# Kernel optimization log

Hardware: AMD Instinct MI355X
Metric: run time of the kernel (lower is better)

The kernel has to match this reference:

```python
import jax, jax.numpy as jnp
import numpy as np

N = 16384   # nodes
E = 524288  # edges (avg degree 32)
D = 32      # input_dim == output_dim


def setup_inputs() -> dict:
    key = jax.random.key(0)
    k_x, k_e, k_wa, k_ba, k_wu, k_bu = jax.random.split(key, 6)
    x = jax.random.normal(k_x, (N, D), dtype=jnp.float32)
    edge_index = jax.random.randint(k_e, (2, E), 0, N, dtype=jnp.int32)
    # nn.Linear init: U(-1/sqrt(fan_in), 1/sqrt(fan_in)), weight shape [out, in]
    bound = 1.0 / np.sqrt(D)
    W_agg = jax.random.uniform(k_wa, (D, D), jnp.float32, -bound, bound)
    b_agg = jax.random.uniform(k_ba, (D,), jnp.float32, -bound, bound)
    W_upd = jax.random.uniform(k_wu, (D, D), jnp.float32, -bound, bound)
    b_upd = jax.random.uniform(k_bu, (D,), jnp.float32, -bound, bound)
    return {"x": x, "edge_index": edge_index, "W_agg": W_agg, "b_agg": b_agg,
            "W_upd": W_upd, "b_upd": b_upd}


def reference(x, edge_index, W_agg, b_agg, W_upd, b_upd):
    n = x.shape[0]
    src, dst = edge_index[0], edge_index[1]
    # Dense symmetric 0/1 adjacency, exactly as the torch module builds it
    # (duplicate edges still write 1 via .set, matching index_put semantics).
    adj = jnp.zeros((n, n), dtype=x.dtype)
    adj = adj.at[src, dst].set(1.0)
    adj = adj.at[dst, src].set(1.0)
    messages = adj @ x                              # [N, D]
    aggregated = messages @ W_agg.T + b_agg         # aggregate_fn(messages)
    updated = x @ W_upd.T + b_upd + aggregated      # update_fn(x) + aggregated
    return updated
```

## Files before the change

kernel.cpp:

```cpp
#include <hip/hip_runtime.h>

#define D 32
#define GCAP 256

__global__ void gnn_edge_bits(const int* __restrict__ src,
                              const int* __restrict__ dst,
                              unsigned int* __restrict__ bm,
                              int E, int wpr) {
    int e = blockIdx.x * blockDim.x + threadIdx.x;
    if (e >= E) return;
    int s = src[e];
    int d = dst[e];
    atomicOr(&bm[(size_t)d * wpr + (s >> 5)], 1u << (s & 31));
    atomicOr(&bm[(size_t)s * wpr + (d >> 5)], 1u << (d & 31));
}

__global__ __launch_bounds__(256) void gnn_gather_update(
        const unsigned int* __restrict__ bm,
        const float* __restrict__ x,
        float* __restrict__ out,
        const float* __restrict__ W_agg,
        const float* __restrict__ b_agg,
        const float* __restrict__ W_upd,
        const float* __restrict__ b_upd,
        int wpr) {
    __shared__ float sWa[D][D + 1];
    __shared__ float sWu[D][D + 1];
    __shared__ float sbias[D];
    __shared__ float sx[16][D];
    __shared__ float sm[16][D];
    __shared__ int   slist[4][4][GCAP];

    int t = threadIdx.x;
    for (int i = t; i < D * D; i += 256) {
        sWa[i >> 5][i & 31] = W_agg[i];
        sWu[i >> 5][i & 31] = W_upd[i];
    }
    if (t < D) sbias[t] = b_agg[t] + b_upd[t];
    for (int i = t; i < 16 * D; i += 256)
        ((float*)sx)[i] = x[(size_t)blockIdx.x * 16 * D + i];

    int lane = t & 63;
    int wv   = t >> 6;
    int dim  = lane & 31;
    int half = lane >> 5;
    int nb   = blockIdx.x * 16 + wv * 4;

    uint4 q[8];
#pragma unroll
    for (int nn = 0; nn < 4; ++nn) {
        const uint4* row = (const uint4*)(bm + (size_t)(nb + nn) * wpr);
        q[nn * 2 + 0] = row[lane];
        q[nn * 2 + 1] = row[64 + lane];
    }

    float accs[4];
#pragma unroll
    for (int nn = 0; nn < 4; ++nn) {
        unsigned int w[8] = { q[nn*2].x,   q[nn*2].y,   q[nn*2].z,   q[nn*2].w,
                              q[nn*2+1].x, q[nn*2+1].y, q[nn*2+1].z, q[nn*2+1].w };
        int myc = 0;
#pragma unroll
        for (int k = 0; k < 8; ++k) myc += __popc(w[k]);
        int pre = myc;
#pragma unroll
        for (int off = 1; off < 64; off <<= 1) {
            int v = __shfl_up(pre, off, 64);
            if (lane >= off) pre += v;
        }
        int total = __shfl(pre, 63, 64);
        pre -= myc;

        float acc = 0.f;
        if (total <= GCAP) {
            int p = pre;
#pragma unroll
            for (int k = 0; k < 8; ++k) {
                unsigned int ww = w[k];
                int widx = (k < 4) ? (4 * lane + k) : (256 + 4 * lane + k - 4);
                int base = widx * 32;
                while (ww) {
                    int b = __ffs(ww) - 1;
                    ww &= ww - 1;
                    slist[wv][nn][p++] = base + b;
                }
            }
            __asm__ __volatile__("s_waitcnt lgkmcnt(0)" ::: "memory");

            const int* sl = slist[wv][nn];
            int j = half;
            for (; j + 16 <= total; j += 16) {
                int c0 = sl[j +  0], c1 = sl[j +  2], c2 = sl[j +  4], c3 = sl[j +  6];
                int c4 = sl[j +  8], c5 = sl[j + 10], c6 = sl[j + 12], c7 = sl[j + 14];
                float v0 = x[(size_t)c0 * D + dim];
                float v1 = x[(size_t)c1 * D + dim];
                float v2 = x[(size_t)c2 * D + dim];
                float v3 = x[(size_t)c3 * D + dim];
                float v4 = x[(size_t)c4 * D + dim];
                float v5 = x[(size_t)c5 * D + dim];
                float v6 = x[(size_t)c6 * D + dim];
                float v7 = x[(size_t)c7 * D + dim];
                acc += v0; acc += v1; acc += v2; acc += v3;
                acc += v4; acc += v5; acc += v6; acc += v7;
            }
            for (; j < total; j += 2)
                acc += x[(size_t)sl[j] * D + dim];
        } else {
#pragma unroll
            for (int k = 0; k < 8; ++k) {
                unsigned long long m = __ballot(w[k] != 0);
                while (m) {
                    int l = __ffsll(m) - 1;
                    m &= m - 1;
                    unsigned int ww = __shfl(w[k], l, 64);
                    int widx = (k < 4) ? (4 * l + k) : (256 + 4 * l + k - 4);
                    int base = widx * 32;
                    while (ww) {
                        int b = __ffs(ww) - 1;
                        ww &= ww - 1;
                        acc += x[(size_t)(base + b) * D + dim];
                    }
                }
            }
        }
        accs[nn] = acc;
    }

#pragma unroll
    for (int nn = 0; nn < 4; ++nn) {
        float a = accs[nn] + __shfl_xor(accs[nn], 32, 64);
        if (lane < D) sm[wv * 4 + nn][lane] = a;
    }
    __syncthreads();

    for (int o = t; o < 16 * D; o += 256) {
        int nl = o >> 5, od = o & 31;
        float r = sbias[od];
#pragma unroll
        for (int k = 0; k < D; ++k)
            r += sx[nl][k] * sWu[od][k] + sm[nl][k] * sWa[od][k];
        out[((size_t)blockIdx.x * 16 + nl) * D + od] = r;
    }
}

#define HASH_BITS 20
#define HASH_SIZE (1u << HASH_BITS)
#define EMPTY_KEY 0xFFFFFFFFu

__global__ void gnn_edge_scatter(const int* __restrict__ src,
                                 const int* __restrict__ dst,
                                 const float* __restrict__ x,
                                 float* __restrict__ msg,
                                 unsigned int* __restrict__ htab, int E, int N) {
    int e = blockIdx.x * blockDim.x + threadIdx.x;
    if (e >= E) return;
    int s = src[e], d = dst[e];
    int a = s < d ? s : d, b = s < d ? d : s;
    unsigned long long key = (unsigned long long)a * N + b;
    unsigned int k32 = (unsigned int)(key & 0xFFFFFFFEu) | 1u;
    unsigned int h = ((unsigned int)key * 2654435761u) >> (32 - HASH_BITS);
    bool inserted;
    for (;;) {
        unsigned int prev = atomicCAS(&htab[h], EMPTY_KEY, k32);
        if (prev == EMPTY_KEY) { inserted = true; break; }
        if (prev == k32)       { inserted = false; break; }
        h = (h + 1) & (HASH_SIZE - 1);
    }
    if (!inserted) return;
    const float* xs = x + (size_t)s * D;
    const float* xd = x + (size_t)d * D;
    if (s == d) {
        float* m = msg + (size_t)s * D;
#pragma unroll
        for (int i = 0; i < D; ++i) atomicAdd(&m[i], xs[i]);
    } else {
        float* ms = msg + (size_t)s * D;
        float* md = msg + (size_t)d * D;
#pragma unroll
        for (int i = 0; i < D; ++i) {
            atomicAdd(&ms[i], xd[i]);
            atomicAdd(&md[i], xs[i]);
        }
    }
}

__global__ __launch_bounds__(256) void gnn_update(
        const float* __restrict__ x, float* __restrict__ out,
        const float* __restrict__ W_agg, const float* __restrict__ b_agg,
        const float* __restrict__ W_upd, const float* __restrict__ b_upd) {
    __shared__ float sWa[D][D + 1], sWu[D][D + 1], sb[D];
    __shared__ float sx[8][D], sm[8][D];
    int t = threadIdx.x;
    for (int i = t; i < D * D; i += 256) {
        sWa[i >> 5][i & 31] = W_agg[i];
        sWu[i >> 5][i & 31] = W_upd[i];
    }
    if (t < D) sb[t] = b_agg[t] + b_upd[t];
    int g = t >> 5, o = t & 31;
    size_t node = (size_t)blockIdx.x * 8 + g;
    sx[g][o] = x[node * D + o];
    sm[g][o] = out[node * D + o];
    __syncthreads();
    float acc = sb[o];
#pragma unroll
    for (int k = 0; k < D; ++k)
        acc += sx[g][k] * sWu[o][k] + sm[g][k] * sWa[o][k];
    out[node * D + o] = acc;
}


extern "C" void kernel_launch(void* const* d_in, const int* in_sizes, int n_in,
                              void* d_out, int out_size, void* d_ws, size_t ws_size,
                              hipStream_t stream) {
    const float* x     = (const float*)d_in[0];
    const int*   eidx  = (const int*)d_in[1];
    const float* W_agg = (const float*)d_in[2];
    const float* b_agg = (const float*)d_in[3];
    const float* W_upd = (const float*)d_in[4];
    const float* b_upd = (const float*)d_in[5];
    float* out = (float*)d_out;

    const int E = in_sizes[1] / 2;
    const int N = in_sizes[0] / D;
    const int* src = eidx;
    const int* dst = eidx + E;

    const int wpr = N >> 5;
    const size_t bm_bytes = (size_t)N * wpr * sizeof(unsigned int);

    if ((N & 15) == 0 && ws_size >= bm_bytes) {
        unsigned int* bm = (unsigned int*)d_ws;
        hipMemsetAsync(bm, 0, bm_bytes, stream);
        gnn_edge_bits<<<(E + 255) / 256, 256, 0, stream>>>(src, dst, bm, E, wpr);
        gnn_gather_update<<<N / 16, 256, 0, stream>>>(bm, x, out, W_agg, b_agg,
                                                      W_upd, b_upd, wpr);
    } else {
        unsigned int* htab = (unsigned int*)d_ws;
        hipMemsetAsync(out, 0, (size_t)N * D * sizeof(float), stream);
        hipMemsetAsync(htab, 0xFF, (size_t)HASH_SIZE * sizeof(unsigned int), stream);
        gnn_edge_scatter<<<(E + 255) / 256, 256, 0, stream>>>(src, dst, x, out,
                                                              htab, E, N);
        gnn_update<<<N / 8, 256, 0, stream>>>(x, out, W_agg, b_agg, W_upd, b_upd);
    }
}
```

Before: 147.2 us.

## Fuse bitmap zero, edge scatter and gather into one cooperative kernel

Replaces the memset plus two kernel launches with a single cooperative kernel of 1024 blocks. It zeroes the adjacency bitmap, sets the edge bits with atomics, then gathers and applies the update, using grid-wide syncs between phases. The goal is to remove launch gaps and the memset. In exchange it adds grid barrier costs and fixes the grid size, which must fit co-resident on the device (N hardcoded to 16384). It also reworks the fallback path into smaller 4-node blocks.

```diff
diff --git a/kernel.cpp b/kernel.cpp
--- a/kernel.cpp
+++ b/kernel.cpp
@@ -1,60 +1,67 @@
 #include <hip/hip_runtime.h>
+#include <hip/hip_cooperative_groups.h>
+
+namespace cg = cooperative_groups;
 
 #define D 32
 #define GCAP 256
-
-__global__ void gnn_edge_bits(const int* __restrict__ src,
-                              const int* __restrict__ dst,
-                              unsigned int* __restrict__ bm,
-                              int E, int wpr) {
-    int e = blockIdx.x * blockDim.x + threadIdx.x;
-    if (e >= E) return;
-    int s = src[e];
-    int d = dst[e];
-    atomicOr(&bm[(size_t)d * wpr + (s >> 5)], 1u << (s & 31));
-    atomicOr(&bm[(size_t)s * wpr + (d >> 5)], 1u << (d & 31));
-}
-
-__global__ __launch_bounds__(256) void gnn_gather_update(
-        const unsigned int* __restrict__ bm,
-        const float* __restrict__ x,
-        float* __restrict__ out,
-        const float* __restrict__ W_agg,
-        const float* __restrict__ b_agg,
-        const float* __restrict__ W_upd,
-        const float* __restrict__ b_upd,
-        int wpr) {
-    __shared__ float sWa[D][D + 1];
-    __shared__ float sWu[D][D + 1];
-    __shared__ float sbias[D];
-    __shared__ float sx[16][D];
-    __shared__ float sm[16][D];
-    __shared__ int   slist[4][4][GCAP];
+#define FBLK 1024
+#define FTHR 256
+
+__global__ __launch_bounds__(FTHR, 4) void gnn_fused(
+        const int* __restrict__ src, const int* __restrict__ dst, int E,
+        unsigned int* __restrict__ bm, int wpr, int nwords,
+        const float* __restrict__ x, float* __restrict__ out,
+        const float* __restrict__ W_agg, const float* __restrict__ b_agg,
+        const float* __restrict__ W_upd, const float* __restrict__ b_upd) {
+    cg::grid_group grid = cg::this_grid();
+
+    __shared__ float sWa[D][D + 1], sWu[D][D + 1], sbias[D];
+    __shared__ float sx[16][D], sm[16][D];
+    __shared__ int   slist[4][GCAP];
 
     int t = threadIdx.x;
-    for (int i = t; i < D * D; i += 256) {
+    int gtid = blockIdx.x * FTHR + t;
+    const int T = FBLK * FTHR;
+
+    for (int i = t; i < D * D; i += FTHR) {
         sWa[i >> 5][i & 31] = W_agg[i];
         sWu[i >> 5][i & 31] = W_upd[i];
     }
     if (t < D) sbias[t] = b_agg[t] + b_upd[t];
-    for (int i = t; i < 16 * D; i += 256)
-        ((float*)sx)[i] = x[(size_t)blockIdx.x * 16 * D + i];
-
-    int lane = t & 63;
-    int wv   = t >> 6;
-    int dim  = lane & 31;
-    int half = lane >> 5;
-    int nb   = blockIdx.x * 16 + wv * 4;
+
+    uint4* bm4 = (uint4*)bm;
+    int nq = nwords >> 2;
+    uint4 z = make_uint4(0u, 0u, 0u, 0u);
+    for (int i = gtid; i < nq; i += T) bm4[i] = z;
+
+    __threadfence();
+    grid.sync();
+
+    for (int e = gtid; e < E; e += T) {
+        int s = src[e], d2 = dst[e];
+        atomicOr(&bm[(size_t)d2 * wpr + (s >> 5)], 1u << (s & 31));
+        atomicOr(&bm[(size_t)s * wpr + (d2 >> 5)], 1u << (d2 & 31));
+    }
+
+    __threadfence();
+    grid.sync();
+    __threadfence();
+
+    int lane = t & 63, wv = t >> 6, dim = lane & 31, half = lane >> 5;
+    int nb0 = blockIdx.x * 16;
+
+    for (int i = t; i < 16 * D; i += FTHR)
+        ((float*)sx)[i] = x[(size_t)nb0 * D + i];
 
     uint4 q[8];
 #pragma unroll
     for (int nn = 0; nn < 4; ++nn) {
-        const uint4* row = (const uint4*)(bm + (size_t)(nb + nn) * wpr);
-        q[nn * 2 + 0] = row[lane];
-        q[nn * 2 + 1] = row[64 + lane];
-    }
-
-    float accs[4];
+        const uint4* row4 = (const uint4*)(bm + (size_t)(nb0 + wv * 4 + nn) * wpr);
+        q[nn * 2 + 0] = row4[lane];
+        q[nn * 2 + 1] = row4[64 + lane];
+    }
+
 #pragma unroll
     for (int nn = 0; nn < 4; ++nn) {
         unsigned int w[8] = { q[nn*2].x,   q[nn*2].y,   q[nn*2].z,   q[nn*2].w,
@@ -82,12 +89,12 @@
                 while (ww) {
                     int b = __ffs(ww) - 1;
                     ww &= ww - 1;
-                    slist[wv][nn][p++] = base + b;
+                    slist[wv][p++] = base + b;
                 }
             }
             __asm__ __volatile__("s_waitcnt lgkmcnt(0)" ::: "memory");
 
-            const int* sl = slist[wv][nn];
+            const int* sl = slist[wv];
             int j = half;
             for (; j + 16 <= total; j += 16) {
                 int c0 = sl[j +  0], c1 = sl[j +  2], c2 = sl[j +  4], c3 = sl[j +  6];
@@ -123,24 +130,129 @@
                 }
             }
         }
-        accs[nn] = acc;
-    }
-
-#pragma unroll
-    for (int nn = 0; nn < 4; ++nn) {
-        float a = accs[nn] + __shfl_xor(accs[nn], 32, 64);
-        if (lane < D) sm[wv * 4 + nn][lane] = a;
+        acc += __shfl_xor(acc, 32, 64);
+        if (lane < D) sm[wv * 4 + nn][lane] = acc;
     }
     __syncthreads();
 
-    for (int o = t; o < 16 * D; o += 256) {
+    for (int o = t; o < 16 * D; o += FTHR) {
         int nl = o >> 5, od = o & 31;
         float r = sbias[od];
 #pragma unroll
         for (int k = 0; k < D; ++k)
             r += sx[nl][k] * sWu[od][k] + sm[nl][k] * sWa[od][k];
-        out[((size_t)blockIdx.x * 16 + nl) * D + od] = r;
-    }
+        out[((size_t)nb0 + nl) * D + od] = r;
+    }
+}
+
+__global__ void gnn_edge_bits(const int* __restrict__ src,
+                              const int* __restrict__ dst,
+                              unsigned int* __restrict__ bm,
+                              int E, int wpr) {
+    int e = blockIdx.x * blockDim.x + threadIdx.x;
+    if (e >= E) return;
+    int s = src[e];
+    int d = dst[e];
+    atomicOr(&bm[(size_t)d * wpr + (s >> 5)], 1u << (s & 31));
+    atomicOr(&bm[(size_t)s * wpr + (d >> 5)], 1u << (d & 31));
+}
+
+__global__ __launch_bounds__(256) void gnn_gather_update(
+        const unsigned int* __restrict__ bm,
+        const float* __restrict__ x,
+        float* __restrict__ out,
+        const float* __restrict__ W_agg,
+        const float* __restrict__ b_agg,
+        const float* __restrict__ W_upd,
+        const float* __restrict__ b_upd,
+        int wpr) {
+    __shared__ float sWa[D][D + 1];
+    __shared__ float sWu[D][D + 1];
+    __shared__ float sb[D];
+    __shared__ float sx[4][D];
+    __shared__ float sm[4][D];
+    __shared__ int   slist[4][384];
+
+    int t = threadIdx.x;
+    for (int i = t; i < D * D; i += 256) {
+        sWa[i >> 5][i & 31] = W_agg[i];
+        sWu[i >> 5][i & 31] = W_upd[i];
+    }
+    if (t < D) sb[t] = b_agg[t] + b_upd[t];
+
+    int lane = t & 63, wv = t >> 6, dim = lane & 31, half = lane >> 5;
+    size_t node = (size_t)blockIdx.x * 4 + wv;
+    if (lane < D) sx[wv][lane] = x[node * D + lane];
+
+    const unsigned int* row = bm + node * (size_t)wpr;
+    unsigned int wb[8];
+#pragma unroll
+    for (int c = 0; c < 8; ++c) wb[c] = row[c * 64 + lane];
+
+    int myc = 0;
+#pragma unroll
+    for (int c = 0; c < 8; ++c) myc += __popc(wb[c]);
+    int pre = myc;
+#pragma unroll
+    for (int off = 1; off < 64; off <<= 1) {
+        int v = __shfl_up(pre, off, 64);
+        if (lane >= off) pre += v;
+    }
+    int total = __shfl(pre, 63, 64);
+    pre -= myc;
+
+    float acc = 0.f;
+    if (total <= 384) {
+        int p = pre;
+#pragma unroll
+        for (int c = 0; c < 8; ++c) {
+            unsigned int ww = wb[c];
+            int base = (c * 64 + lane) * 32;
+            while (ww) { int b = __ffs(ww) - 1; ww &= ww - 1; slist[wv][p++] = base + b; }
+        }
+        __asm__ __volatile__("s_waitcnt lgkmcnt(0)" ::: "memory");
+        int j = half;
+        for (; j + 8 <= total; j += 8) {
+            int c0 = slist[wv][j + 0], c1 = slist[wv][j + 2];
+            int c2 = slist[wv][j + 4], c3 = slist[wv][j + 6];
+            float v0 = x[(size_t)c0 * D + dim];
+            float v1 = x[(size_t)c1 * D + dim];
+            float v2 = x[(size_t)c2 * D + dim];
+            float v3 = x[(size_t)c3 * D + dim];
+            acc += v0; acc += v1; acc += v2; acc += v3;
+        }
+        for (; j < total; j += 2) acc += x[(size_t)slist[wv][j] * D + dim];
+    } else {
+        for (int c = 0; c < 8; ++c) {
+            unsigned long long m = __ballot(wb[c] != 0);
+            while (m) {
+                int l = __ffsll(m) - 1; m &= m - 1;
+                unsigned int ww = __shfl(wb[c], l, 64);
+                int base = (c * 64 + l) * 32;
+                while (ww) { int b = __ffs(ww) - 1; ww &= ww - 1;
+                             acc += x[(size_t)(base + b) * D + dim]; }
+            }
+        }
+    }
+    acc += __shfl_xor(acc, 32, 64);
+    if (lane < D) sm[wv][lane] = acc;
+    __syncthreads();
+
+    if (t < 128) {
+        int ns = t >> 5, o = t & 31;
+        float r = sb[o];
+#pragma unroll
+        for (int k = 0; k < D; ++k)
+            r += sx[ns][k] * sWu[o][k] + sm[ns][k] * sWa[o][k];
+        out[((size_t)blockIdx.x * 4 + ns) * D + o] = r;
+    }
+}
+
+__global__ void gnn_zero(uint4* p, int nq) {
+    int i = blockIdx.x * blockDim.x + threadIdx.x;
+    int T = gridDim.x * blockDim.x;
+    uint4 z = make_uint4(0u, 0u, 0u, 0u);
+    for (; i < nq; i += T) p[i] = z;
 }
 
 #define HASH_BITS 20
@@ -220,20 +332,31 @@
     const float* b_upd = (const float*)d_in[5];
     float* out = (float*)d_out;
 
-    const int E = in_sizes[1] / 2;
-    const int N = in_sizes[0] / D;
+    int E = in_sizes[1] / 2;
+    int N = in_sizes[0] / D;
     const int* src = eidx;
     const int* dst = eidx + E;
 
-    const int wpr = N >> 5;
-    const size_t bm_bytes = (size_t)N * wpr * sizeof(unsigned int);
-
-    if ((N & 15) == 0 && ws_size >= bm_bytes) {
+    int wpr = N >> 5;
+    int nwords = N * wpr;
+    size_t bm_bytes = (size_t)nwords * sizeof(unsigned int);
+
+    if (N == 16384 && ws_size >= bm_bytes) {
         unsigned int* bm = (unsigned int*)d_ws;
-        hipMemsetAsync(bm, 0, bm_bytes, stream);
+        void* args[] = { (void*)&src, (void*)&dst, (void*)&E,
+                         (void*)&bm, (void*)&wpr, (void*)&nwords,
+                         (void*)&x, (void*)&out,
+                         (void*)&W_agg, (void*)&b_agg,
+                         (void*)&W_upd, (void*)&b_upd };
+        hipError_t err = hipLaunchCooperativeKernel((const void*)gnn_fused,
+                                                    dim3(FBLK), dim3(FTHR),
+                                                    args, 0, stream);
+        if (err == hipSuccess) return;
+
+        gnn_zero<<<2048, 256, 0, stream>>>((uint4*)bm, nwords >> 2);
         gnn_edge_bits<<<(E + 255) / 256, 256, 0, stream>>>(src, dst, bm, E, wpr);
-        gnn_gather_update<<<N / 16, 256, 0, stream>>>(bm, x, out, W_agg, b_agg,
-                                                      W_upd, b_upd, wpr);
+        gnn_gather_update<<<N / 4, 256, 0, stream>>>(bm, x, out, W_agg, b_agg,
+                                                     W_upd, b_upd, wpr);
     } else {
         unsigned int* htab = (unsigned int*)d_ws;
         hipMemsetAsync(out, 0, (size_t)N * D * sizeof(float), stream);
```

After: 543.1 us. 3.69x slower.
